# Performance work log

Hardware: AMD Instinct MI355X
Metric: run time of the kernel (lower is better)

The kernel has to match this reference:

```python
import jax, jax.numpy as jnp
import numpy as np

N = 256          # args.image_size
B = 64           # args.batch_size
K = 5            # args.kernel_size
RHO = 1
ETA = 1.0
IDEN_OFF = 4.0   # identity_offset
DEF_OFF = (2.0 + IDEN_OFF / (N - 1)) / 2.0   # deforming_offset
SCALE = IDEN_OFF / (N - 1)


def _iden_grid():
    # torch.arange(-(N-1), N, 2) / (N-1): N values from -1 to 1
    seq = jnp.arange(-(N - 1), N, 2) / (N - 1.0)
    gx = jnp.broadcast_to(seq[None, :], (N, N))   # x varies along width
    return jnp.stack([gx, gx.T], 0)[None]          # [1,2,N,N]


def _gauss2d():
    sigma = K * 0.15 + 0.35
    half = (K - 1) * 0.5
    x = jnp.linspace(-half, half, K)
    pdf = jnp.exp(-0.5 * (x / sigma) ** 2)
    k1 = pdf / pdf.sum()
    return jnp.outer(k1, k1)                        # [K,K]


def _forward(image, prim_grid):
    Bsz = prim_grid.shape[0]
    # --- gaussian_blur: reflect pad + depthwise conv ---
    pad = K // 2
    pg = jnp.pad(prim_grid, ((0, 0), (0, 0), (pad, pad), (pad, pad)), mode='reflect')
    kern = jnp.broadcast_to(_gauss2d(), (2, 1, K, K))
    pg = jax.lax.conv_general_dilated(
        pg, kern, (1, 1), 'VALID',
        dimension_numbers=('NCHW', 'OIHW', 'NCHW'), feature_group_count=2)
    iden = _iden_grid()
    # --- prim -> samp, samp -> accu (the [1,-1] conv_transpose == shifted diff) ---
    s = pg + iden + DEF_OFF                           # [B,2,N,N]
    sx, sy = s[:, 0], s[:, 1]
    zx = jnp.zeros((Bsz, N, 1), sx.dtype)
    zy = jnp.zeros((Bsz, 1, N), sy.dtype)
    accu_x = (sx - jnp.concatenate([zx, sx[:, :, :-1]], axis=2)) / SCALE
    accu_y = (sy - jnp.concatenate([zy, sy[:, :-1, :]], axis=1)) / SCALE
    # --- accu_clip ---
    accu_x = jax.nn.relu(accu_x)
    accu_y = jax.nn.relu(accu_y)
    # --- accu -> samp (all-ones-kernel conv_transpose == cumsum) ---
    samp_x = jnp.cumsum(accu_x * SCALE, axis=2) - DEF_OFF
    samp_y = jnp.cumsum(accu_y * SCALE, axis=1) - DEF_OFF
    samp = jnp.stack([samp_x, samp_y], 1)             # [B,2,N,N]
    # --- prim_clip then samp_clip ---
    pw = 2.0 / N
    prim = jnp.clip(samp - iden, -pw * RHO, pw * RHO)
    samp = jnp.clip(prim + iden, -ETA, ETA)
    # --- grid_sample: bilinear, align_corners=True, zeros padding ---
    gx, gy = samp[:, 0], samp[:, 1]                   # [B,N,N]
    Himg, Wimg = image.shape[2], image.shape[3]
    ix = (gx + 1.0) * 0.5 * (Wimg - 1)
    iy = (gy + 1.0) * 0.5 * (Himg - 1)
    x0 = jnp.floor(ix)
    y0 = jnp.floor(iy)
    wx1 = ix - x0
    wy1 = iy - y0
    b = jnp.arange(Bsz)[:, None, None]

    def corner(xc, yc):
        valid = ((xc >= 0) & (xc <= Wimg - 1) & (yc >= 0) & (yc <= Himg - 1)).astype(image.dtype)
        xi = jnp.clip(xc, 0, Wimg - 1).astype(jnp.int32)
        yi = jnp.clip(yc, 0, Himg - 1).astype(jnp.int32)
        return image[b, :, yi, xi] * valid[..., None]   # [B,N,N,C]

    out = (corner(x0, y0) * ((1 - wx1) * (1 - wy1))[..., None]
           + corner(x0 + 1, y0) * (wx1 * (1 - wy1))[..., None]
           + corner(x0, y0 + 1) * ((1 - wx1) * wy1)[..., None]
           + corner(x0 + 1, y0 + 1) * (wx1 * wy1)[..., None])
    return jnp.transpose(out, (0, 3, 1, 2))            # [B,C,N,N]


def setup_inputs() -> dict:
    key = jax.random.key(0)
    k1, k2 = jax.random.split(key)
    image = jax.random.normal(k1, (B, 3, N, N), dtype=jnp.float32)
    prim_grid = jax.random.normal(k2, (B, 2, N, N), dtype=jnp.float32)
    return {"image": image, "prim_grid": prim_grid}


def reference(image, prim_grid):
    return _forward(image, prim_grid)
```

## Files before the change

### kernel.cpp

```cpp
#include <hip/hip_runtime.h>

namespace {

constexpr int Nn = 256;
constexpr int Bn = 64;
constexpr int SEG = 8;
constexpr int NSEG = Nn / SEG;

constexpr float KW0 = 0.07076638f;
constexpr float KW1 = 0.24446039f;
constexpr float KW2 = 0.36954646f;

constexpr float DEF_OFF   = 1.00784313725490196f;
constexpr float SCALE     = 0.01568627450980392f;
constexpr float INV_SCALE = 63.75f;
constexpr float TWO255    = 0.00784313725490196f;
constexpr float PW        = 0.0078125f;

__device__ __forceinline__ int reflN(int i) {
    if (i < 0) i = -i;
    if (i >= Nn) i = 2 * (Nn - 1) - i;
    return i;
}

__device__ __forceinline__ float seqf(int t) {
    return (float)(2 * t - (Nn - 1)) * (1.0f / (float)(Nn - 1));
}

__device__ __forceinline__ void segb(int lin, int& seg, int& b) {
    int wg = (lin & 7) * 256 + (lin >> 3);
    seg = wg & (NSEG - 1);
    b = wg >> 5;
}

__global__ __launch_bounds__(256) void kA_kernel(const float* __restrict__ prim,
                                                 float* __restrict__ gx_out,
                                                 float* __restrict__ accu_out,
                                                 float* __restrict__ partial) {
    const int j = threadIdx.x;
    int seg, b;
    segb(blockIdx.x, seg, b);
    const int i0 = seg * SEG;

    const float* c0 = prim + (size_t)b * 2 * Nn * Nn;
    const float* c1 = c0 + (size_t)Nn * Nn;

    float a0[12], a1[13];
    #pragma unroll
    for (int t = 0; t < 12; ++t) a0[t] = c0[reflN(i0 - 2 + t) * Nn + j];
    #pragma unroll
    for (int t = 0; t < 13; ++t) a1[t] = c1[reflN(i0 - 3 + t) * Nn + j];

    __shared__ float vb[17][Nn];
    __shared__ float wsum[SEG][4];

    #pragma unroll
    for (int r = 0; r < 8; ++r)
        vb[r][j] = KW0 * (a0[r] + a0[r + 4]) + KW1 * (a0[r + 1] + a0[r + 3]) + KW2 * a0[r + 2];
    #pragma unroll
    for (int r = 0; r < 9; ++r)
        vb[8 + r][j] = KW0 * (a1[r] + a1[r + 4]) + KW1 * (a1[r + 1] + a1[r + 3]) + KW2 * a1[r + 2];
    __syncthreads();

    const int jm3 = reflN(j - 3), jm2 = reflN(j - 2), jm1 = reflN(j - 1),
              jp1 = reflN(j + 1), jp2 = reflN(j + 2);
    const int lane = j & 63;
    const int wave = j >> 6;

    float val[SEG];
    #pragma unroll
    for (int r = 0; r < 8; ++r) {
        const float* v = vb[r];
        float h  = KW0 * (v[jm2] + v[jp2]) + KW1 * (v[jm1] + v[jp1]) + KW2 * v[j];
        float hm = KW0 * (v[jm3] + v[jp1]) + KW1 * (v[jm2] + v[j])   + KW2 * v[jm1];
        if (j == 0) hm = 0.0f;
        float accu = fmaxf((h - hm + TWO255) * INV_SCALE, 0.0f);
        float s = accu;
        #pragma unroll
        for (int off = 1; off < 64; off <<= 1) {
            float u = __shfl_up(s, off, 64);
            if (lane >= off) s += u;
        }
        val[r] = s;
        if (lane == 63) wsum[r][wave] = s;
    }
    __syncthreads();

    const float sq_j = seqf(j);
    #pragma unroll
    for (int r = 0; r < 8; ++r) {
        float add = 0.0f;
        for (int w = 0; w < wave; ++w) add += wsum[r][w];
        float samp = (val[r] + add) * SCALE - DEF_OFF;
        float p = fminf(fmaxf(samp - sq_j, -PW), PW);
        float g = fminf(fmaxf(p + sq_j, -1.0f), 1.0f);
        gx_out[((size_t)b * Nn + i0 + r) * Nn + j] = g;
    }

    float h1[9];
    #pragma unroll
    for (int r = 0; r < 9; ++r) {
        const float* v = vb[8 + r];
        h1[r] = KW0 * (v[jm2] + v[jp2]) + KW1 * (v[jm1] + v[jp1]) + KW2 * v[j];
    }
    float psum = 0.0f;
    #pragma unroll
    for (int rr = 0; rr < 8; ++rr) {
        float hm = (rr == 0 && seg == 0) ? 0.0f : h1[rr];
        float acc = fmaxf((h1[rr + 1] - hm + TWO255) * INV_SCALE, 0.0f);
        accu_out[((size_t)b * Nn + i0 + rr) * Nn + j] = acc;
        psum += acc;
    }
    partial[((size_t)b * NSEG + seg) * Nn + j] = psum;
}

__global__ __launch_bounds__(256) void k3_kernel(const float* __restrict__ accu,
                                                 const float* __restrict__ partial,
                                                 const float* __restrict__ gx_buf,
                                                 const float* __restrict__ image,
                                                 float* __restrict__ outp) {
    const int j = threadIdx.x;
    int seg, b;
    segb(blockIdx.x, seg, b);
    const int i0 = seg * SEG;

    const float* pb = partial + (size_t)b * NSEG * Nn + j;
    float carry = 0.0f;
    #pragma unroll
    for (int k = 0; k < NSEG - 1; ++k) {
        float p = pb[(size_t)k * Nn];
        carry += (k < seg) ? p : 0.0f;
    }

    float av[SEG], gxv[SEG];
    #pragma unroll
    for (int k = 0; k < SEG; ++k) av[k] = accu[((size_t)b * Nn + i0 + k) * Nn + j];
    #pragma unroll
    for (int k = 0; k < SEG; ++k) gxv[k] = gx_buf[((size_t)b * Nn + i0 + k) * Nn + j];

    float wxs[SEG], wys[SEG];
    int x0s[SEG], y0s[SEG];
    float cum = carry;
    #pragma unroll
    for (int k = 0; k < SEG; ++k) {
        const int i = i0 + k;
        cum += av[k];
        float samp = cum * SCALE - DEF_OFF;
        float sq = seqf(i);
        float p  = fminf(fmaxf(samp - sq, -PW), PW);
        float gy = fminf(fmaxf(p + sq, -1.0f), 1.0f);
        float ix = (gxv[k] + 1.0f) * 127.5f;
        float iy = (gy + 1.0f) * 127.5f;
        float xf = floorf(ix), yf = floorf(iy);
        wxs[k] = ix - xf; wys[k] = iy - yf;
        x0s[k] = (int)xf; y0s[k] = (int)yf;
    }

    __shared__ float tile[10 * Nn];
    for (int c = 0; c < 3; ++c) {
        if (c) __syncthreads();
        const float* img = image + (size_t)(b * 3 + c) * Nn * Nn;
        #pragma unroll
        for (int r = 0; r < 10; ++r) {
            int row = min(max(i0 - 1 + r, 0), Nn - 1);
            tile[r * Nn + j] = img[row * Nn + j];
        }
        __syncthreads();
        #pragma unroll
        for (int k = 0; k < SEG; ++k) {
            int x0 = x0s[k], y0 = y0s[k];
            float wx1 = wxs[k], wy1 = wys[k];
            float wx0 = 1.0f - wx1, wy0 = 1.0f - wy1;
            bool vx0 = x0 >= 0, vx1 = x0 < Nn - 1;
            bool vy0 = y0 >= 0, vy1 = y0 < Nn - 1;
            int x0c = max(x0, 0), x1c = min(x0 + 1, Nn - 1);
            int ly0 = max(y0, 0) - i0 + 1;
            int ly1 = min(y0 + 1, Nn - 1) - i0 + 1;
            float w00 = (vx0 && vy0) ? wx0 * wy0 : 0.0f;
            float w10 = (vx1 && vy0) ? wx1 * wy0 : 0.0f;
            float w01 = (vx0 && vy1) ? wx0 * wy1 : 0.0f;
            float w11 = (vx1 && vy1) ? wx1 * wy1 : 0.0f;
            float v = w00 * tile[ly0 * Nn + x0c] + w10 * tile[ly0 * Nn + x1c]
                    + w01 * tile[ly1 * Nn + x0c] + w11 * tile[ly1 * Nn + x1c];
            __builtin_nontemporal_store(v, &outp[(((size_t)b * 3 + c) * Nn + (i0 + k)) * Nn + j]);
        }
    }
}

}

extern "C" void kernel_launch(void* const* d_in, const int* in_sizes, int n_in,
                              void* d_out, int out_size, void* d_ws, size_t ws_size,
                              hipStream_t stream) {
    const float* image = (const float*)d_in[0];
    const float* prim  = (const float*)d_in[1];
    float* outp = (float*)d_out;

    float* gx_buf   = (float*)d_ws;
    float* accu_buf = gx_buf + (size_t)Bn * Nn * Nn;
    float* partial  = accu_buf + (size_t)Bn * Nn * Nn;

    kA_kernel<<<NSEG * Bn, 256, 0, stream>>>(prim, gx_buf, accu_buf, partial);
    k3_kernel<<<NSEG * Bn, 256, 0, stream>>>(accu_buf, partial, gx_buf, image, outp);
}
```

Baseline: 42.65 us.

## Recompute blur in final kernel instead of storing gx/accu intermediates

The first kernel now computes only the per-segment column partial sums of the y-channel accumulation. The second kernel re-reads prim, redoes the blur, the x-direction scan and the y cumsum, then performs grid sampling. This removes the full-size gx and accu intermediate buffers, which were written once and read once through global memory. In exchange prim's y channel is read and blurred twice. The segment size also goes from 8 to 16 rows, the image tile load uses float4, and bounds checks are dropped where the clamp to [-1,1] already guarantees validity.

```diff
diff --git a/kernel.cpp b/kernel.cpp
--- a/kernel.cpp
+++ b/kernel.cpp
@@ -4,7 +4,7 @@
 
 constexpr int Nn = 256;
 constexpr int Bn = 64;
-constexpr int SEG = 8;
+constexpr int SEG = 16;
 constexpr int NSEG = Nn / SEG;
 
 constexpr float KW0 = 0.07076638f;
@@ -28,160 +28,176 @@
 }
 
 __device__ __forceinline__ void segb(int lin, int& seg, int& b) {
-    int wg = (lin & 7) * 256 + (lin >> 3);
+    int wg = (lin & 7) * 128 + (lin >> 3);
+    b = wg >> 4;
     seg = wg & (NSEG - 1);
-    b = wg >> 5;
-}
-
-__global__ __launch_bounds__(256) void kA_kernel(const float* __restrict__ prim,
-                                                 float* __restrict__ gx_out,
-                                                 float* __restrict__ accu_out,
-                                                 float* __restrict__ partial) {
+}
+
+__global__ __launch_bounds__(256, 4) void kP_kernel(const float* __restrict__ prim,
+                                                    float* __restrict__ partial) {
     const int j = threadIdx.x;
     int seg, b;
     segb(blockIdx.x, seg, b);
     const int i0 = seg * SEG;
+    const float* c1 = prim + ((size_t)b * 2 + 1) * Nn * Nn;
+
+    float a[SEG + 5];
+    #pragma unroll
+    for (int t = 0; t < SEG + 5; ++t) a[t] = c1[reflN(i0 - 3 + t) * Nn + j];
+
+    __shared__ float vb[(SEG + 1) * Nn];
+    #pragma unroll
+    for (int r = 0; r < SEG + 1; ++r)
+        vb[r * Nn + j] = KW0 * (a[r] + a[r + 4]) + KW1 * (a[r + 1] + a[r + 3]) + KW2 * a[r + 2];
+    __syncthreads();
+
+    const int jm2 = reflN(j - 2), jm1 = reflN(j - 1), jp1 = reflN(j + 1), jp2 = reflN(j + 2);
+    auto hc = [&](const float* v) {
+        return KW0 * (v[jm2] + v[jp2]) + KW1 * (v[jm1] + v[jp1]) + KW2 * v[j];
+    };
+
+    float hprev = hc(&vb[0]);
+    float psum = 0.0f;
+    #pragma unroll
+    for (int r = 0; r < SEG; ++r) {
+        float h = hc(&vb[(r + 1) * Nn]);
+        float hm = (r == 0 && seg == 0) ? 0.0f : hprev;
+        psum += fmaxf((h - hm + TWO255) * INV_SCALE, 0.0f);
+        hprev = h;
+    }
+    partial[((size_t)b * NSEG + seg) * Nn + j] = psum;
+}
+
+__global__ __launch_bounds__(256, 4) void kF_kernel(const float* __restrict__ prim,
+                                                    const float* __restrict__ image,
+                                                    const float* __restrict__ partial,
+                                                    float* __restrict__ outp) {
+    const int j = threadIdx.x;
+    int seg, b;
+    segb(blockIdx.x, seg, b);
+    const int i0 = seg * SEG;
 
     const float* c0 = prim + (size_t)b * 2 * Nn * Nn;
     const float* c1 = c0 + (size_t)Nn * Nn;
 
-    float a0[12], a1[13];
-    #pragma unroll
-    for (int t = 0; t < 12; ++t) a0[t] = c0[reflN(i0 - 2 + t) * Nn + j];
-    #pragma unroll
-    for (int t = 0; t < 13; ++t) a1[t] = c1[reflN(i0 - 3 + t) * Nn + j];
-
-    __shared__ float vb[17][Nn];
+    __shared__ float vb[(SEG + 2) * Nn];
     __shared__ float wsum[SEG][4];
 
-    #pragma unroll
-    for (int r = 0; r < 8; ++r)
-        vb[r][j] = KW0 * (a0[r] + a0[r + 4]) + KW1 * (a0[r + 1] + a0[r + 3]) + KW2 * a0[r + 2];
-    #pragma unroll
-    for (int r = 0; r < 9; ++r)
-        vb[8 + r][j] = KW0 * (a1[r] + a1[r + 4]) + KW1 * (a1[r + 1] + a1[r + 3]) + KW2 * a1[r + 2];
-    __syncthreads();
+    const float* pb = partial + (size_t)b * NSEG * Nn + j;
+    float carry = 0.0f;
+    #pragma unroll
+    for (int k = 0; k < NSEG - 1; ++k) {
+        float p = pb[(size_t)k * Nn];
+        carry += (k < seg) ? p : 0.0f;
+    }
 
     const int jm3 = reflN(j - 3), jm2 = reflN(j - 2), jm1 = reflN(j - 1),
               jp1 = reflN(j + 1), jp2 = reflN(j + 2);
     const int lane = j & 63;
     const int wave = j >> 6;
-
-    float val[SEG];
-    #pragma unroll
-    for (int r = 0; r < 8; ++r) {
-        const float* v = vb[r];
-        float h  = KW0 * (v[jm2] + v[jp2]) + KW1 * (v[jm1] + v[jp1]) + KW2 * v[j];
-        float hm = KW0 * (v[jm3] + v[jp1]) + KW1 * (v[jm2] + v[j])   + KW2 * v[jm1];
-        if (j == 0) hm = 0.0f;
-        float accu = fmaxf((h - hm + TWO255) * INV_SCALE, 0.0f);
-        float s = accu;
-        #pragma unroll
-        for (int off = 1; off < 64; off <<= 1) {
-            float u = __shfl_up(s, off, 64);
-            if (lane >= off) s += u;
-        }
-        val[r] = s;
-        if (lane == 63) wsum[r][wave] = s;
-    }
-    __syncthreads();
-
-    const float sq_j = seqf(j);
-    #pragma unroll
-    for (int r = 0; r < 8; ++r) {
-        float add = 0.0f;
-        for (int w = 0; w < wave; ++w) add += wsum[r][w];
-        float samp = (val[r] + add) * SCALE - DEF_OFF;
-        float p = fminf(fmaxf(samp - sq_j, -PW), PW);
-        float g = fminf(fmaxf(p + sq_j, -1.0f), 1.0f);
-        gx_out[((size_t)b * Nn + i0 + r) * Nn + j] = g;
-    }
-
-    float h1[9];
-    #pragma unroll
-    for (int r = 0; r < 9; ++r) {
-        const float* v = vb[8 + r];
-        h1[r] = KW0 * (v[jm2] + v[jp2]) + KW1 * (v[jm1] + v[jp1]) + KW2 * v[j];
-    }
-    float psum = 0.0f;
-    #pragma unroll
-    for (int rr = 0; rr < 8; ++rr) {
-        float hm = (rr == 0 && seg == 0) ? 0.0f : h1[rr];
-        float acc = fmaxf((h1[rr + 1] - hm + TWO255) * INV_SCALE, 0.0f);
-        accu_out[((size_t)b * Nn + i0 + rr) * Nn + j] = acc;
-        psum += acc;
-    }
-    partial[((size_t)b * NSEG + seg) * Nn + j] = psum;
-}
-
-__global__ __launch_bounds__(256) void k3_kernel(const float* __restrict__ accu,
-                                                 const float* __restrict__ partial,
-                                                 const float* __restrict__ gx_buf,
-                                                 const float* __restrict__ image,
-                                                 float* __restrict__ outp) {
-    const int j = threadIdx.x;
-    int seg, b;
-    segb(blockIdx.x, seg, b);
-    const int i0 = seg * SEG;
-
-    const float* pb = partial + (size_t)b * NSEG * Nn + j;
-    float carry = 0.0f;
-    #pragma unroll
-    for (int k = 0; k < NSEG - 1; ++k) {
-        float p = pb[(size_t)k * Nn];
-        carry += (k < seg) ? p : 0.0f;
-    }
-
-    float av[SEG], gxv[SEG];
-    #pragma unroll
-    for (int k = 0; k < SEG; ++k) av[k] = accu[((size_t)b * Nn + i0 + k) * Nn + j];
-    #pragma unroll
-    for (int k = 0; k < SEG; ++k) gxv[k] = gx_buf[((size_t)b * Nn + i0 + k) * Nn + j];
-
-    float wxs[SEG], wys[SEG];
-    int x0s[SEG], y0s[SEG];
-    float cum = carry;
-    #pragma unroll
-    for (int k = 0; k < SEG; ++k) {
-        const int i = i0 + k;
-        cum += av[k];
-        float samp = cum * SCALE - DEF_OFF;
-        float sq = seqf(i);
-        float p  = fminf(fmaxf(samp - sq, -PW), PW);
-        float gy = fminf(fmaxf(p + sq, -1.0f), 1.0f);
-        float ix = (gxv[k] + 1.0f) * 127.5f;
-        float iy = (gy + 1.0f) * 127.5f;
-        float xf = floorf(ix), yf = floorf(iy);
-        wxs[k] = ix - xf; wys[k] = iy - yf;
-        x0s[k] = (int)xf; y0s[k] = (int)yf;
-    }
-
-    __shared__ float tile[10 * Nn];
+    auto hc = [&](const float* v) {
+        return KW0 * (v[jm2] + v[jp2]) + KW1 * (v[jm1] + v[jp1]) + KW2 * v[j];
+    };
+
+    float accu[SEG];
+    {
+        float a[SEG + 5];
+        #pragma unroll
+        for (int t = 0; t < SEG + 5; ++t) a[t] = c1[reflN(i0 - 3 + t) * Nn + j];
+        #pragma unroll
+        for (int r = 0; r < SEG + 1; ++r)
+            vb[r * Nn + j] = KW0 * (a[r] + a[r + 4]) + KW1 * (a[r + 1] + a[r + 3]) + KW2 * a[r + 2];
+        __syncthreads();
+        float hprev = hc(&vb[0]);
+        #pragma unroll
+        for (int r = 0; r < SEG; ++r) {
+            float h = hc(&vb[(r + 1) * Nn]);
+            float hm = (r == 0 && seg == 0) ? 0.0f : hprev;
+            accu[r] = fmaxf((h - hm + TWO255) * INV_SCALE, 0.0f);
+            hprev = h;
+        }
+        __syncthreads();
+    }
+
+    float ix[SEG];
+    {
+        float a[SEG + 4];
+        #pragma unroll
+        for (int t = 0; t < SEG + 4; ++t) a[t] = c0[reflN(i0 - 2 + t) * Nn + j];
+        #pragma unroll
+        for (int r = 0; r < SEG; ++r)
+            vb[r * Nn + j] = KW0 * (a[r] + a[r + 4]) + KW1 * (a[r + 1] + a[r + 3]) + KW2 * a[r + 2];
+        __syncthreads();
+        #pragma unroll
+        for (int r = 0; r < SEG; ++r) {
+            const float* v = &vb[r * Nn];
+            float h  = hc(v);
+            float hm = KW0 * (v[jm3] + v[jp1]) + KW1 * (v[jm2] + v[j]) + KW2 * v[jm1];
+            if (j == 0) hm = 0.0f;
+            float s = fmaxf((h - hm + TWO255) * INV_SCALE, 0.0f);
+            #pragma unroll
+            for (int off = 1; off < 64; off <<= 1) {
+                float u = __shfl_up(s, off, 64);
+                if (lane >= off) s += u;
+            }
+            ix[r] = s;
+            if (lane == 63) wsum[r][wave] = s;
+        }
+        __syncthreads();
+        const float sq_j = seqf(j);
+        #pragma unroll
+        for (int r = 0; r < SEG; ++r) {
+            float add = 0.0f;
+            for (int w = 0; w < wave; ++w) add += wsum[r][w];
+            float samp = (ix[r] + add) * SCALE - DEF_OFF;
+            float p = fminf(fmaxf(samp - sq_j, -PW), PW);
+            float g = fminf(fmaxf(p + sq_j, -1.0f), 1.0f);
+            ix[r] = (g + 1.0f) * 127.5f;
+        }
+    }
+
+    float iy[SEG];
+    {
+        float cum = carry;
+        #pragma unroll
+        for (int k = 0; k < SEG; ++k) {
+            cum += accu[k];
+            float samp = cum * SCALE - DEF_OFF;
+            float sq = seqf(i0 + k);
+            float p  = fminf(fmaxf(samp - sq, -PW), PW);
+            float gy = fminf(fmaxf(p + sq, -1.0f), 1.0f);
+            iy[k] = (gy + 1.0f) * 127.5f;
+        }
+    }
+
     for (int c = 0; c < 3; ++c) {
         if (c) __syncthreads();
         const float* img = image + (size_t)(b * 3 + c) * Nn * Nn;
         #pragma unroll
-        for (int r = 0; r < 10; ++r) {
-            int row = min(max(i0 - 1 + r, 0), Nn - 1);
-            tile[r * Nn + j] = img[row * Nn + j];
+        for (int q = 0; q < 5; ++q) {
+            int r = q * 4 + (j >> 6);
+            if (r < SEG + 2) {
+                int row = min(max(i0 - 1 + r, 0), Nn - 1);
+                ((float4*)&vb[r * Nn])[j & 63] = ((const float4*)(img + row * Nn))[j & 63];
+            }
         }
         __syncthreads();
         #pragma unroll
         for (int k = 0; k < SEG; ++k) {
-            int x0 = x0s[k], y0 = y0s[k];
-            float wx1 = wxs[k], wy1 = wys[k];
+            float fx = floorf(ix[k]), fy = floorf(iy[k]);
+            int x0 = (int)fx, y0 = (int)fy;
+            float wx1 = ix[k] - fx, wy1 = iy[k] - fy;
             float wx0 = 1.0f - wx1, wy0 = 1.0f - wy1;
-            bool vx0 = x0 >= 0, vx1 = x0 < Nn - 1;
-            bool vy0 = y0 >= 0, vy1 = y0 < Nn - 1;
-            int x0c = max(x0, 0), x1c = min(x0 + 1, Nn - 1);
-            int ly0 = max(y0, 0) - i0 + 1;
+            bool vx1 = x0 < Nn - 1, vy1 = y0 < Nn - 1;
+            int x0c = x0, x1c = min(x0 + 1, Nn - 1);
+            int ly0 = y0 - i0 + 1;
             int ly1 = min(y0 + 1, Nn - 1) - i0 + 1;
-            float w00 = (vx0 && vy0) ? wx0 * wy0 : 0.0f;
-            float w10 = (vx1 && vy0) ? wx1 * wy0 : 0.0f;
-            float w01 = (vx0 && vy1) ? wx0 * wy1 : 0.0f;
+            float w00 = wx0 * wy0;
+            float w10 = vx1 ? wx1 * wy0 : 0.0f;
+            float w01 = vy1 ? wx0 * wy1 : 0.0f;
             float w11 = (vx1 && vy1) ? wx1 * wy1 : 0.0f;
-            float v = w00 * tile[ly0 * Nn + x0c] + w10 * tile[ly0 * Nn + x1c]
-                    + w01 * tile[ly1 * Nn + x0c] + w11 * tile[ly1 * Nn + x1c];
+            float v = w00 * vb[ly0 * Nn + x0c] + w10 * vb[ly0 * Nn + x1c]
+                    + w01 * vb[ly1 * Nn + x0c] + w11 * vb[ly1 * Nn + x1c];
             __builtin_nontemporal_store(v, &outp[(((size_t)b * 3 + c) * Nn + (i0 + k)) * Nn + j]);
         }
     }
@@ -195,11 +211,8 @@
     const float* image = (const float*)d_in[0];
     const float* prim  = (const float*)d_in[1];
     float* outp = (float*)d_out;
-
-    float* gx_buf   = (float*)d_ws;
-    float* accu_buf = gx_buf + (size_t)Bn * Nn * Nn;
-    float* partial  = accu_buf + (size_t)Bn * Nn * Nn;
-
-    kA_kernel<<<NSEG * Bn, 256, 0, stream>>>(prim, gx_buf, accu_buf, partial);
-    k3_kernel<<<NSEG * Bn, 256, 0, stream>>>(accu_buf, partial, gx_buf, image, outp);
-}
+    float* partial = (float*)d_ws;
+
+    kP_kernel<<<NSEG * Bn, 256, 0, stream>>>(prim, partial);
+    kF_kernel<<<NSEG * Bn, 256, 0, stream>>>(prim, image, partial, outp);
+}
```

New measurement: 66.81 us. +56.6%, slower.
